# Optimization experiments

Measured on AMD Instinct MI355X. Metric: run time of the kernel, lower is better.

Reference implementation:

```python
import jax, jax.numpy as jnp
import numpy as np

N_GROUP = 8
TOPK_GROUP = 4
TOP_K = 8
ROUTED_SCALING_FACTOR = 2.5
RENORMALIZE = True


def setup_inputs() -> dict:
    key = jax.random.key(0)
    k1, k2 = jax.random.split(key)
    num_tokens, n_experts = 131072, 256
    router_logits = jax.random.normal(k1, (num_tokens, n_experts), dtype=jnp.float32)
    e_score_correction_bias = jax.random.normal(k2, (n_experts,), dtype=jnp.float32) * 0.1
    return {"router_logits": router_logits,
            "e_score_correction_bias": e_score_correction_bias}


def reference(router_logits, e_score_correction_bias):
    T, E = router_logits.shape
    per_group = E // N_GROUP  # 32 experts per group

    # sigmoid scoring + bias correction (bias used for selection only)
    scores = jax.nn.sigmoid(router_logits)                      # [T, E]
    scores_for_choice = scores + e_score_correction_bias[None, :]

    # group score = sum of top-2 corrected scores within each group
    grouped = scores_for_choice.reshape(T, N_GROUP, per_group)  # [T, G, E/G]
    top2_vals, _ = jax.lax.top_k(grouped, 2)                    # [T, G, 2]
    group_scores = top2_vals.sum(axis=-1)                       # [T, G]

    # pick topk_group groups, build expert-level mask
    _, group_idx = jax.lax.top_k(group_scores, TOPK_GROUP)      # [T, topk_group]
    group_mask = jnp.zeros((T, N_GROUP), dtype=jnp.bool_)
    group_mask = group_mask.at[jnp.arange(T)[:, None], group_idx].set(True)
    score_mask = jnp.repeat(group_mask, per_group, axis=1)      # [T, E]

    # mask non-selected groups, then global top-k over remaining experts
    masked_scores = jnp.where(score_mask, scores_for_choice, 0.0)
    _, topk_ids = jax.lax.top_k(masked_scores, TOP_K)           # [T, top_k]

    # gather UNcorrected sigmoid scores as weights
    topk_weights = jnp.take_along_axis(scores, topk_ids, axis=1)  # [T, top_k]
    if RENORMALIZE:
        topk_weights = topk_weights / (topk_weights.sum(axis=-1, keepdims=True) + 1e-20)
    topk_weights = topk_weights * ROUTED_SCALING_FACTOR
    return topk_weights, topk_ids
```

## Files before the change

kernel.cpp:

```cpp
#include <hip/hip_runtime.h>
#include <math.h>

#define THREADS 256
#define TPB 32
#define NEXP 256
#define Q_EPS  12u
#define QG_EPS 28u

__device__ __forceinline__ float fsigmoid(float x) {
    float e = __expf(-x);
    return __fdividef(1.0f, 1.0f + e);
}

__device__ __forceinline__ double dsigmoid(float xf) {
    xf = fminf(fmaxf(xf, -500.0f), 500.0f);
    double x = (double)xf;
    double t = x * -1.4426950408889634074;
    double n = floor(t + 0.5);
    int ni = (int)n;
    double u = (t - n) * 0.69314718055994530942;
    double pp = 2.08767569878680990e-9;
    pp = fma(pp, u, 2.50521083854417188e-8);
    pp = fma(pp, u, 2.75573192239858907e-7);
    pp = fma(pp, u, 2.75573192239858883e-6);
    pp = fma(pp, u, 2.48015873015873016e-5);
    pp = fma(pp, u, 1.98412698412698413e-4);
    pp = fma(pp, u, 1.38888888888888889e-3);
    pp = fma(pp, u, 8.33333333333333333e-3);
    pp = fma(pp, u, 4.16666666666666667e-2);
    pp = fma(pp, u, 1.66666666666666667e-1);
    pp = fma(pp, u, 0.5);
    pp = fma(pp, u, 1.0);
    pp = fma(pp, u, 1.0);
    double sc = __longlong_as_double((long long)(1023 + ni) << 52);
    double e = pp * sc;
    double w = 1.0 + e;
    double y = (double)__fdividef(1.0f, (float)w);
    y = fma(y, fma(-w, y, 1.0), y);
    y = fma(y, fma(-w, y, 1.0), y);
    return y;
}

#define DINS(cc, ee) do {                                                \
    double _d=(cc); int _e=(ee);                                         \
    if (_d > s7) {                                                       \
        bool _b0=_d>s0,_b1=_d>s1,_b2=_d>s2,_b3=_d>s3,_b4=_d>s4,          \
             _b5=_d>s5,_b6=_d>s6;                                        \
        s7=_b6?s6:_d;           c7=_b6?c6:_e;                            \
        s6=_b5?s5:(_b6?_d:s6);  c6=_b5?c5:(_b6?_e:c6);                   \
        s5=_b4?s4:(_b5?_d:s5);  c5=_b4?c4:(_b5?_e:c5);                   \
        s4=_b3?s3:(_b4?_d:s4);  c4=_b3?c3:(_b4?_e:c4);                   \
        s3=_b2?s2:(_b3?_d:s3);  c3=_b2?c2:(_b3?_e:c3);                   \
        s2=_b1?s1:(_b2?_d:s2);  c2=_b1?c1:(_b2?_e:c2);                   \
        s1=_b0?s0:(_b1?_d:s1);  c1=_b0?c0:(_b1?_e:c1);                   \
        s0=_b0?_d:s0;           c0=_b0?_e:c0;                            \
    } } while (0)


#define CEU(a, b) do {                                                   \
    unsigned _x=(a), _y=(b);                                             \
    (a) = _x>_y ? _x : _y; (b) = _x>_y ? _y : _x;                        \
} while (0)
#define VMU(a, b) do { (a) = (a)>(b) ? (a) : (b); } while (0)

#define SORT8U(v0,v1,v2,v3,v4,v5,v6,v7) do {                             \
    CEU(v0,v1); CEU(v2,v3); CEU(v4,v5); CEU(v6,v7);                      \
    CEU(v0,v2); CEU(v1,v3); CEU(v4,v6); CEU(v5,v7);                      \
    CEU(v1,v2); CEU(v5,v6);                                              \
    CEU(v0,v4); CEU(v1,v5); CEU(v2,v6); CEU(v3,v7);                      \
    CEU(v2,v4); CEU(v3,v5);                                              \
    CEU(v1,v2); CEU(v3,v4); CEU(v5,v6);                                  \
} while (0)

#define CLEAN9M(a0,a1,a2,a3,a4,a5,a6,a7,a8) do {                         \
    CEU(a0,a8);                                                          \
    CEU(a1,a5); CEU(a2,a6); CEU(a3,a7); CEU(a4,a8);                      \
    CEU(a1,a3); CEU(a2,a4); CEU(a5,a7); CEU(a6,a8);                      \
    CEU(a1,a2); CEU(a3,a4); CEU(a5,a6); CEU(a7,a8);                      \
} while (0)

#define XMERGE_U(d) do {                                                 \
    unsigned q0=(unsigned)__shfl_xor((int)m0,d,64),                      \
             q1=(unsigned)__shfl_xor((int)m1,d,64),                      \
             q2=(unsigned)__shfl_xor((int)m2,d,64),                      \
             q3=(unsigned)__shfl_xor((int)m3,d,64),                      \
             q4=(unsigned)__shfl_xor((int)m4,d,64),                      \
             q5=(unsigned)__shfl_xor((int)m5,d,64),                      \
             q6=(unsigned)__shfl_xor((int)m6,d,64),                      \
             q7=(unsigned)__shfl_xor((int)m7,d,64),                      \
             q8=(unsigned)__shfl_xor((int)m8,d,64);                      \
    VMU(m0,q8); VMU(m1,q7); VMU(m2,q6); VMU(m3,q5); VMU(m4,q4);          \
    VMU(m5,q3); VMU(m6,q2); VMU(m7,q1); VMU(m8,q0);                      \
    CLEAN9M(m0,m1,m2,m3,m4,m5,m6,m7,m8);                                 \
} while (0)

__global__ __launch_bounds__(THREADS, 4)
void noauxtc_router_kernel(const float* __restrict__ logits,
                           const float* __restrict__ bias,
                           float* __restrict__ out,
                           int T)
{
    __shared__ __align__(16) float bias_sh[NEXP];
    __shared__ __align__(16) float biasq_sh[NEXP];

    const int tid   = threadIdx.x;
    const int h     = tid & 7;
    const int p     = tid >> 3;
    const int tok0  = blockIdx.x * TPB;
    const int token = tok0 + p;
    const int lane  = tid & 63;
    const int base  = lane & 56;

    const float4* lg4 = (const float4*)logits;
    float4 st[8];
    #pragma unroll
    for (int k = 0; k < 8; ++k)
        st[k] = lg4[(size_t)token * 64 + h * 8 + k];

    {
        float b = bias[tid];
        bias_sh[tid]  = b;
        biasq_sh[tid] = fmaf(b, 4194304.0f, 2097152.0f);
    }
    __syncthreads();

    const float4* bq4 = (const float4*)biasq_sh;

    unsigned kk[32];
    #pragma unroll
    for (int q = 0; q < 8; ++q) {
        float4 Bq = bq4[h * 8 + q];
        float4 x  = st[q];
        int idf = 255 - (h * 32 + q * 4);
        kk[q*4+0] = ((unsigned)fmaf(fsigmoid(x.x), 4194304.0f, Bq.x) << 8) + (unsigned)(idf    );
        kk[q*4+1] = ((unsigned)fmaf(fsigmoid(x.y), 4194304.0f, Bq.y) << 8) + (unsigned)(idf - 1);
        kk[q*4+2] = ((unsigned)fmaf(fsigmoid(x.z), 4194304.0f, Bq.z) << 8) + (unsigned)(idf - 2);
        kk[q*4+3] = ((unsigned)fmaf(fsigmoid(x.w), 4194304.0f, Bq.w) << 8) + (unsigned)(idf - 3);
    }

    SORT8U(kk[0], kk[1], kk[2], kk[3], kk[4], kk[5], kk[6], kk[7]);
    SORT8U(kk[8], kk[9], kk[10],kk[11],kk[12],kk[13],kk[14],kk[15]);
    SORT8U(kk[16],kk[17],kk[18],kk[19],kk[20],kk[21],kk[22],kk[23]);
    SORT8U(kk[24],kk[25],kk[26],kk[27],kk[28],kk[29],kk[30],kk[31]);

    unsigned t0=kk[0],t1=kk[1],t2=kk[2],t3=kk[3],t4=kk[4],t5=kk[5],t6=kk[6],t7=kk[7],t8=0u;
    VMU(t1,kk[15]); VMU(t2,kk[14]); VMU(t3,kk[13]); VMU(t4,kk[12]);
    VMU(t5,kk[11]); VMU(t6,kk[10]); VMU(t7,kk[9]);  VMU(t8,kk[8]);
    CLEAN9M(t0,t1,t2,t3,t4,t5,t6,t7,t8);

    unsigned u0=kk[16],u1=kk[17],u2=kk[18],u3=kk[19],u4=kk[20],u5=kk[21],u6=kk[22],u7=kk[23],u8=0u;
    VMU(u1,kk[31]); VMU(u2,kk[30]); VMU(u3,kk[29]); VMU(u4,kk[28]);
    VMU(u5,kk[27]); VMU(u6,kk[26]); VMU(u7,kk[25]); VMU(u8,kk[24]);
    CLEAN9M(u0,u1,u2,u3,u4,u5,u6,u7,u8);

    unsigned m0=t0,m1=t1,m2=t2,m3=t3,m4=t4,m5=t5,m6=t6,m7=t7,m8=t8;
    VMU(m0,u8); VMU(m1,u7); VMU(m2,u6); VMU(m3,u5); VMU(m4,u4);
    VMU(m5,u3); VMU(m6,u2); VMU(m7,u1); VMU(m8,u0);
    CLEAN9M(m0,m1,m2,m3,m4,m5,m6,m7,m8);

    unsigned gq   = (m0 >> 8) + (m1 >> 8);
    unsigned gkey = (gq << 3) + (unsigned)(7 - h);

    unsigned gk0 = (unsigned)__shfl((int)gkey, base + 0, 64);
    unsigned gk1 = (unsigned)__shfl((int)gkey, base + 1, 64);
    unsigned gk2 = (unsigned)__shfl((int)gkey, base + 2, 64);
    unsigned gk3 = (unsigned)__shfl((int)gkey, base + 3, 64);
    unsigned gk4 = (unsigned)__shfl((int)gkey, base + 4, 64);
    unsigned gk5 = (unsigned)__shfl((int)gkey, base + 5, 64);
    unsigned gk6 = (unsigned)__shfl((int)gkey, base + 6, 64);
    unsigned gk7 = (unsigned)__shfl((int)gkey, base + 7, 64);
    SORT8U(gk0,gk1,gk2,gk3,gk4,gk5,gk6,gk7);

    int selmask = (1 << ((gk0 & 7u) ^ 7u)) | (1 << ((gk1 & 7u) ^ 7u)) |
                  (1 << ((gk2 & 7u) ^ 7u)) | (1 << ((gk3 & 7u) ^ 7u));

    if (__builtin_expect((gk3 >> 3) - (gk4 >> 3) < QG_EPS, 0)) {
        double a1 = -1e300, a2 = -1e300;
        const float* lgp = logits + (size_t)token * 256 + h * 32;
        #pragma unroll 1
        for (int k = 0; k < 32; ++k) {
            double c = dsigmoid(lgp[k]) + (double)bias_sh[h * 32 + k];
            a2 = fmax(a2, fmin(a1, c)); a1 = fmax(a1, c);
        }
        double gdo = a1 + a2;
        double gd[8];
        #pragma unroll
        for (int g = 0; g < 8; ++g) gd[g] = __shfl(gdo, base + g, 64);
        int sm = 0;
        #pragma unroll
        for (int a = 0; a < 8; ++a) {
            int rk = 0;
            #pragma unroll
            for (int b = 0; b < 8; ++b) {
                if (b == a) continue;
                bool beat = (b < a) ? (gd[b] >= gd[a]) : (gd[b] > gd[a]);
                rk += beat ? 1 : 0;
            }
            sm |= (rk < 4) ? (1 << a) : 0;
        }
        selmask = sm;
    }

    {
        bool sel = (selmask >> h) & 1;
        m0 = sel ? m0 : 0u; m1 = sel ? m1 : 0u; m2 = sel ? m2 : 0u;
        m3 = sel ? m3 : 0u; m4 = sel ? m4 : 0u; m5 = sel ? m5 : 0u;
        m6 = sel ? m6 : 0u; m7 = sel ? m7 : 0u; m8 = sel ? m8 : 0u;
    }

    XMERGE_U(1);
    XMERGE_U(2);
    XMERGE_U(4);

    unsigned q0=m0>>8, q1=m1>>8, q2=m2>>8, q3=m3>>8, q4=m4>>8,
             q5=m5>>8, q6=m6>>8, q7=m7>>8, q8=m8>>8;
    int n0=255-(int)(m0&255u), n1=255-(int)(m1&255u), n2=255-(int)(m2&255u),
        n3=255-(int)(m3&255u), n4=255-(int)(m4&255u), n5=255-(int)(m5&255u),
        n6=255-(int)(m6&255u), n7=255-(int)(m7&255u), n8=255-(int)(m8&255u);

    const float QS = 2.384185791015625e-7f;
    float v0=(float)q0*QS-0.5f, v1=(float)q1*QS-0.5f, v2=(float)q2*QS-0.5f,
          v3=(float)q3*QS-0.5f, v4=(float)q4*QS-0.5f, v5=(float)q5*QS-0.5f,
          v6=(float)q6*QS-0.5f, v7=(float)q7*QS-0.5f;

    float w0 = v0 - bias_sh[n0], w1 = v1 - bias_sh[n1], w2 = v2 - bias_sh[n2],
          w3 = v3 - bias_sh[n3], w4 = v4 - bias_sh[n4], w5 = v5 - bias_sh[n5],
          w6 = v6 - bias_sh[n6], w7 = v7 - bias_sh[n7];
    int o0=n0,o1=n1,o2=n2,o3=n3,o4=n4,o5=n5,o6=n6,o7=n7;

    bool flagB = (h == 0) &&
                 ((q0-q1<Q_EPS)|(q1-q2<Q_EPS)|(q2-q3<Q_EPS)|(q3-q4<Q_EPS)|
                  (q4-q5<Q_EPS)|(q5-q6<Q_EPS)|(q6-q7<Q_EPS)|(q7-q8<Q_EPS));
    if (__builtin_expect(flagB, 0)) {
        double s0=-1e300,s1=-1e300,s2=-1e300,s3=-1e300,
               s4=-1e300,s5=-1e300,s6=-1e300,s7=-1e300;
        int c0=0,c1=0,c2=0,c3=0,c4=0,c5=0,c6=0,c7=0;
        int ci[9] = {n0,n1,n2,n3,n4,n5,n6,n7,n8};
        const float* lgt = logits + (size_t)token * 256;
        #pragma unroll 1
        for (int k = 0; k < 9; ++k) {
            int e = ci[k];
            double cs = dsigmoid(lgt[e]) + (double)bias_sh[e];
            DINS(cs, e);
        }
        w0=(float)(s0-(double)bias_sh[c0]); o0=c0;
        w1=(float)(s1-(double)bias_sh[c1]); o1=c1;
        w2=(float)(s2-(double)bias_sh[c2]); o2=c2;
        w3=(float)(s3-(double)bias_sh[c3]); o3=c3;
        w4=(float)(s4-(double)bias_sh[c4]); o4=c4;
        w5=(float)(s5-(double)bias_sh[c5]); o5=c5;
        w6=(float)(s6-(double)bias_sh[c6]); o6=c6;
        w7=(float)(s7-(double)bias_sh[c7]); o7=c7;
    }

    if (h == 0) {
        float sum = ((w0+w1)+(w2+w3)) + ((w4+w5)+(w6+w7));
        float scl = 2.5f / (sum + 1e-20f);
        float4 oa, ob;
        oa.x=w0*scl; oa.y=w1*scl; oa.z=w2*scl; oa.w=w3*scl;
        ob.x=w4*scl; ob.y=w5*scl; ob.z=w6*scl; ob.w=w7*scl;
        *(float4*)(out + (size_t)token*8)     = oa;
        *(float4*)(out + (size_t)token*8 + 4) = ob;
        float* oid = out + (size_t)T*8;
        float4 ia, ib;
        ia.x=(float)o0; ia.y=(float)o1; ia.z=(float)o2; ia.w=(float)o3;
        ib.x=(float)o4; ib.y=(float)o5; ib.z=(float)o6; ib.w=(float)o7;
        *(float4*)(oid + (size_t)token*8)     = ia;
        *(float4*)(oid + (size_t)token*8 + 4) = ib;
    }
}

extern "C" void kernel_launch(void* const* d_in, const int* in_sizes, int n_in,
                              void* d_out, int out_size, void* d_ws, size_t ws_size,
                              hipStream_t stream) {
    const float* logits = (const float*)d_in[0];
    const float* bias   = (const float*)d_in[1];
    float* out = (float*)d_out;
    int T = in_sizes[0] / NEXP;
    int nblocks = T / TPB;
    noauxtc_router_kernel<<<nblocks, THREADS, 0, stream>>>(logits, bias, out, T);
}
```

Measured before the change: 200.6 us.

## Process two tokens per thread and drop shared-memory bias staging

Each block now handles 64 tokens, with every thread processing two tokens in sequence. This halves the grid and amortizes the per-block bias setup. The shared-memory bias arrays and the __syncthreads are removed. Each thread instead loads its 32 bias values into registers and prequantizes them once, and final bias lookups come from global memory (likely cached). The trade-offs are that the two tokens are processed serially without overlapping their loads, register pressure rises from holding the bias registers, and the number of blocks in flight drops.

```diff
diff --git a/kernel.cpp b/kernel.cpp
--- a/kernel.cpp
+++ b/kernel.cpp
@@ -2,7 +2,7 @@
 #include <math.h>
 
 #define THREADS 256
-#define TPB 32
+#define TPB 64
 #define NEXP 256
 #define Q_EPS  12u
 #define QG_EPS 28u
@@ -100,174 +100,175 @@
                            float* __restrict__ out,
                            int T)
 {
-    __shared__ __align__(16) float bias_sh[NEXP];
-    __shared__ __align__(16) float biasq_sh[NEXP];
-
     const int tid   = threadIdx.x;
     const int h     = tid & 7;
     const int p     = tid >> 3;
     const int tok0  = blockIdx.x * TPB;
-    const int token = tok0 + p;
     const int lane  = tid & 63;
     const int base  = lane & 56;
 
-    const float4* lg4 = (const float4*)logits;
-    float4 st[8];
+    const float4* bg4 = (const float4*)bias + h * 8;
+    float4 Bq[8];
     #pragma unroll
-    for (int k = 0; k < 8; ++k)
-        st[k] = lg4[(size_t)token * 64 + h * 8 + k];
-
-    {
-        float b = bias[tid];
-        bias_sh[tid]  = b;
-        biasq_sh[tid] = fmaf(b, 4194304.0f, 2097152.0f);
+    for (int j = 0; j < 8; ++j) {
+        float4 b = bg4[j];
+        Bq[j].x = fmaf(b.x, 4194304.0f, 2097152.0f);
+        Bq[j].y = fmaf(b.y, 4194304.0f, 2097152.0f);
+        Bq[j].z = fmaf(b.z, 4194304.0f, 2097152.0f);
+        Bq[j].w = fmaf(b.w, 4194304.0f, 2097152.0f);
     }
-    __syncthreads();
-
-    const float4* bq4 = (const float4*)biasq_sh;
-
-    unsigned kk[32];
-    #pragma unroll
-    for (int q = 0; q < 8; ++q) {
-        float4 Bq = bq4[h * 8 + q];
-        float4 x  = st[q];
-        int idf = 255 - (h * 32 + q * 4);
-        kk[q*4+0] = ((unsigned)fmaf(fsigmoid(x.x), 4194304.0f, Bq.x) << 8) + (unsigned)(idf    );
-        kk[q*4+1] = ((unsigned)fmaf(fsigmoid(x.y), 4194304.0f, Bq.y) << 8) + (unsigned)(idf - 1);
-        kk[q*4+2] = ((unsigned)fmaf(fsigmoid(x.z), 4194304.0f, Bq.z) << 8) + (unsigned)(idf - 2);
-        kk[q*4+3] = ((unsigned)fmaf(fsigmoid(x.w), 4194304.0f, Bq.w) << 8) + (unsigned)(idf - 3);
-    }
-
-    SORT8U(kk[0], kk[1], kk[2], kk[3], kk[4], kk[5], kk[6], kk[7]);
-    SORT8U(kk[8], kk[9], kk[10],kk[11],kk[12],kk[13],kk[14],kk[15]);
-    SORT8U(kk[16],kk[17],kk[18],kk[19],kk[20],kk[21],kk[22],kk[23]);
-    SORT8U(kk[24],kk[25],kk[26],kk[27],kk[28],kk[29],kk[30],kk[31]);
-
-    unsigned t0=kk[0],t1=kk[1],t2=kk[2],t3=kk[3],t4=kk[4],t5=kk[5],t6=kk[6],t7=kk[7],t8=0u;
-    VMU(t1,kk[15]); VMU(t2,kk[14]); VMU(t3,kk[13]); VMU(t4,kk[12]);
-    VMU(t5,kk[11]); VMU(t6,kk[10]); VMU(t7,kk[9]);  VMU(t8,kk[8]);
-    CLEAN9M(t0,t1,t2,t3,t4,t5,t6,t7,t8);
-
-    unsigned u0=kk[16],u1=kk[17],u2=kk[18],u3=kk[19],u4=kk[20],u5=kk[21],u6=kk[22],u7=kk[23],u8=0u;
-    VMU(u1,kk[31]); VMU(u2,kk[30]); VMU(u3,kk[29]); VMU(u4,kk[28]);
-    VMU(u5,kk[27]); VMU(u6,kk[26]); VMU(u7,kk[25]); VMU(u8,kk[24]);
-    CLEAN9M(u0,u1,u2,u3,u4,u5,u6,u7,u8);
-
-    unsigned m0=t0,m1=t1,m2=t2,m3=t3,m4=t4,m5=t5,m6=t6,m7=t7,m8=t8;
-    VMU(m0,u8); VMU(m1,u7); VMU(m2,u6); VMU(m3,u5); VMU(m4,u4);
-    VMU(m5,u3); VMU(m6,u2); VMU(m7,u1); VMU(m8,u0);
-    CLEAN9M(m0,m1,m2,m3,m4,m5,m6,m7,m8);
-
-    unsigned gq   = (m0 >> 8) + (m1 >> 8);
-    unsigned gkey = (gq << 3) + (unsigned)(7 - h);
-
-    unsigned gk0 = (unsigned)__shfl((int)gkey, base + 0, 64);
-    unsigned gk1 = (unsigned)__shfl((int)gkey, base + 1, 64);
-    unsigned gk2 = (unsigned)__shfl((int)gkey, base + 2, 64);
-    unsigned gk3 = (unsigned)__shfl((int)gkey, base + 3, 64);
-    unsigned gk4 = (unsigned)__shfl((int)gkey, base + 4, 64);
-    unsigned gk5 = (unsigned)__shfl((int)gkey, base + 5, 64);
-    unsigned gk6 = (unsigned)__shfl((int)gkey, base + 6, 64);
-    unsigned gk7 = (unsigned)__shfl((int)gkey, base + 7, 64);
-    SORT8U(gk0,gk1,gk2,gk3,gk4,gk5,gk6,gk7);
-
-    int selmask = (1 << ((gk0 & 7u) ^ 7u)) | (1 << ((gk1 & 7u) ^ 7u)) |
-                  (1 << ((gk2 & 7u) ^ 7u)) | (1 << ((gk3 & 7u) ^ 7u));
-
-    if (__builtin_expect((gk3 >> 3) - (gk4 >> 3) < QG_EPS, 0)) {
-        double a1 = -1e300, a2 = -1e300;
-        const float* lgp = logits + (size_t)token * 256 + h * 32;
-        #pragma unroll 1
-        for (int k = 0; k < 32; ++k) {
-            double c = dsigmoid(lgp[k]) + (double)bias_sh[h * 32 + k];
-            a2 = fmax(a2, fmin(a1, c)); a1 = fmax(a1, c);
-        }
-        double gdo = a1 + a2;
-        double gd[8];
+
+    auto process = [&](int token) {
+        const float4* lg4 = (const float4*)logits + (size_t)token * 64 + h * 8;
+        float4 st[8];
         #pragma unroll
-        for (int g = 0; g < 8; ++g) gd[g] = __shfl(gdo, base + g, 64);
-        int sm = 0;
+        for (int k = 0; k < 8; ++k) st[k] = lg4[k];
+
+        unsigned kk[32];
         #pragma unroll
-        for (int a = 0; a < 8; ++a) {
-            int rk = 0;
+        for (int q = 0; q < 8; ++q) {
+            float4 x = st[q], B = Bq[q];
+            int idf = 255 - (h * 32 + q * 4);
+            kk[q*4+0] = ((unsigned)fmaf(fsigmoid(x.x), 4194304.0f, B.x) << 8) + (unsigned)(idf    );
+            kk[q*4+1] = ((unsigned)fmaf(fsigmoid(x.y), 4194304.0f, B.y) << 8) + (unsigned)(idf - 1);
+            kk[q*4+2] = ((unsigned)fmaf(fsigmoid(x.z), 4194304.0f, B.z) << 8) + (unsigned)(idf - 2);
+            kk[q*4+3] = ((unsigned)fmaf(fsigmoid(x.w), 4194304.0f, B.w) << 8) + (unsigned)(idf - 3);
+        }
+
+        SORT8U(kk[0], kk[1], kk[2], kk[3], kk[4], kk[5], kk[6], kk[7]);
+        SORT8U(kk[8], kk[9], kk[10],kk[11],kk[12],kk[13],kk[14],kk[15]);
+        SORT8U(kk[16],kk[17],kk[18],kk[19],kk[20],kk[21],kk[22],kk[23]);
+        SORT8U(kk[24],kk[25],kk[26],kk[27],kk[28],kk[29],kk[30],kk[31]);
+
+        unsigned t0=kk[0],t1=kk[1],t2=kk[2],t3=kk[3],t4=kk[4],t5=kk[5],t6=kk[6],t7=kk[7],t8=0u;
+        VMU(t1,kk[15]); VMU(t2,kk[14]); VMU(t3,kk[13]); VMU(t4,kk[12]);
+        VMU(t5,kk[11]); VMU(t6,kk[10]); VMU(t7,kk[9]);  VMU(t8,kk[8]);
+        CLEAN9M(t0,t1,t2,t3,t4,t5,t6,t7,t8);
+
+        unsigned u0=kk[16],u1=kk[17],u2=kk[18],u3=kk[19],u4=kk[20],u5=kk[21],u6=kk[22],u7=kk[23],u8=0u;
+        VMU(u1,kk[31]); VMU(u2,kk[30]); VMU(u3,kk[29]); VMU(u4,kk[28]);
+        VMU(u5,kk[27]); VMU(u6,kk[26]); VMU(u7,kk[25]); VMU(u8,kk[24]);
+        CLEAN9M(u0,u1,u2,u3,u4,u5,u6,u7,u8);
+
+        unsigned m0=t0,m1=t1,m2=t2,m3=t3,m4=t4,m5=t5,m6=t6,m7=t7,m8=t8;
+        VMU(m0,u8); VMU(m1,u7); VMU(m2,u6); VMU(m3,u5); VMU(m4,u4);
+        VMU(m5,u3); VMU(m6,u2); VMU(m7,u1); VMU(m8,u0);
+        CLEAN9M(m0,m1,m2,m3,m4,m5,m6,m7,m8);
+
+        unsigned gq   = (m0 >> 8) + (m1 >> 8);
+        unsigned gkey = (gq << 3) + (unsigned)(7 - h);
+
+        unsigned gk0 = (unsigned)__shfl((int)gkey, base + 0, 64);
+        unsigned gk1 = (unsigned)__shfl((int)gkey, base + 1, 64);
+        unsigned gk2 = (unsigned)__shfl((int)gkey, base + 2, 64);
+        unsigned gk3 = (unsigned)__shfl((int)gkey, base + 3, 64);
+        unsigned gk4 = (unsigned)__shfl((int)gkey, base + 4, 64);
+        unsigned gk5 = (unsigned)__shfl((int)gkey, base + 5, 64);
+        unsigned gk6 = (unsigned)__shfl((int)gkey, base + 6, 64);
+        unsigned gk7 = (unsigned)__shfl((int)gkey, base + 7, 64);
+        SORT8U(gk0,gk1,gk2,gk3,gk4,gk5,gk6,gk7);
+
+        int selmask = (1 << ((gk0 & 7u) ^ 7u)) | (1 << ((gk1 & 7u) ^ 7u)) |
+                      (1 << ((gk2 & 7u) ^ 7u)) | (1 << ((gk3 & 7u) ^ 7u));
+
+        if (__builtin_expect((gk3 >> 3) - (gk4 >> 3) < QG_EPS, 0)) {
+            double a1 = -1e300, a2 = -1e300;
+            const float* lgp = logits + (size_t)token * 256 + h * 32;
+            const float* bp  = bias + h * 32;
+            #pragma unroll 1
+            for (int k = 0; k < 32; ++k) {
+                double c = dsigmoid(lgp[k]) + (double)bp[k];
+                a2 = fmax(a2, fmin(a1, c)); a1 = fmax(a1, c);
+            }
+            double gdo = a1 + a2;
+            double gd[8];
             #pragma unroll
-            for (int b = 0; b < 8; ++b) {
-                if (b == a) continue;
-                bool beat = (b < a) ? (gd[b] >= gd[a]) : (gd[b] > gd[a]);
-                rk += beat ? 1 : 0;
+            for (int g = 0; g < 8; ++g) gd[g] = __shfl(gdo, base + g, 64);
+            int sm = 0;
+            #pragma unroll
+            for (int a = 0; a < 8; ++a) {
+                int rk = 0;
+                #pragma unroll
+                for (int b = 0; b < 8; ++b) {
+                    if (b == a) continue;
+                    bool beat = (b < a) ? (gd[b] >= gd[a]) : (gd[b] > gd[a]);
+                    rk += beat ? 1 : 0;
+                }
+                sm |= (rk < 4) ? (1 << a) : 0;
             }
-            sm |= (rk < 4) ? (1 << a) : 0;
-        }
-        selmask = sm;
-    }
-
-    {
-        bool sel = (selmask >> h) & 1;
-        m0 = sel ? m0 : 0u; m1 = sel ? m1 : 0u; m2 = sel ? m2 : 0u;
-        m3 = sel ? m3 : 0u; m4 = sel ? m4 : 0u; m5 = sel ? m5 : 0u;
-        m6 = sel ? m6 : 0u; m7 = sel ? m7 : 0u; m8 = sel ? m8 : 0u;
-    }
-
-    XMERGE_U(1);
-    XMERGE_U(2);
-    XMERGE_U(4);
-
-    unsigned q0=m0>>8, q1=m1>>8, q2=m2>>8, q3=m3>>8, q4=m4>>8,
-             q5=m5>>8, q6=m6>>8, q7=m7>>8, q8=m8>>8;
-    int n0=255-(int)(m0&255u), n1=255-(int)(m1&255u), n2=255-(int)(m2&255u),
-        n3=255-(int)(m3&255u), n4=255-(int)(m4&255u), n5=255-(int)(m5&255u),
-        n6=255-(int)(m6&255u), n7=255-(int)(m7&255u), n8=255-(int)(m8&255u);
-
-    const float QS = 2.384185791015625e-7f;
-    float v0=(float)q0*QS-0.5f, v1=(float)q1*QS-0.5f, v2=(float)q2*QS-0.5f,
-          v3=(float)q3*QS-0.5f, v4=(float)q4*QS-0.5f, v5=(float)q5*QS-0.5f,
-          v6=(float)q6*QS-0.5f, v7=(float)q7*QS-0.5f;
-
-    float w0 = v0 - bias_sh[n0], w1 = v1 - bias_sh[n1], w2 = v2 - bias_sh[n2],
-          w3 = v3 - bias_sh[n3], w4 = v4 - bias_sh[n4], w5 = v5 - bias_sh[n5],
-          w6 = v6 - bias_sh[n6], w7 = v7 - bias_sh[n7];
-    int o0=n0,o1=n1,o2=n2,o3=n3,o4=n4,o5=n5,o6=n6,o7=n7;
-
-    bool flagB = (h == 0) &&
-                 ((q0-q1<Q_EPS)|(q1-q2<Q_EPS)|(q2-q3<Q_EPS)|(q3-q4<Q_EPS)|
-                  (q4-q5<Q_EPS)|(q5-q6<Q_EPS)|(q6-q7<Q_EPS)|(q7-q8<Q_EPS));
-    if (__builtin_expect(flagB, 0)) {
-        double s0=-1e300,s1=-1e300,s2=-1e300,s3=-1e300,
-               s4=-1e300,s5=-1e300,s6=-1e300,s7=-1e300;
-        int c0=0,c1=0,c2=0,c3=0,c4=0,c5=0,c6=0,c7=0;
-        int ci[9] = {n0,n1,n2,n3,n4,n5,n6,n7,n8};
-        const float* lgt = logits + (size_t)token * 256;
-        #pragma unroll 1
-        for (int k = 0; k < 9; ++k) {
-            int e = ci[k];
-            double cs = dsigmoid(lgt[e]) + (double)bias_sh[e];
-            DINS(cs, e);
-        }
-        w0=(float)(s0-(double)bias_sh[c0]); o0=c0;
-        w1=(float)(s1-(double)bias_sh[c1]); o1=c1;
-        w2=(float)(s2-(double)bias_sh[c2]); o2=c2;
-        w3=(float)(s3-(double)bias_sh[c3]); o3=c3;
-        w4=(float)(s4-(double)bias_sh[c4]); o4=c4;
-        w5=(float)(s5-(double)bias_sh[c5]); o5=c5;
-        w6=(float)(s6-(double)bias_sh[c6]); o6=c6;
-        w7=(float)(s7-(double)bias_sh[c7]); o7=c7;
-    }
-
-    if (h == 0) {
-        float sum = ((w0+w1)+(w2+w3)) + ((w4+w5)+(w6+w7));
-        float scl = 2.5f / (sum + 1e-20f);
-        float4 oa, ob;
-        oa.x=w0*scl; oa.y=w1*scl; oa.z=w2*scl; oa.w=w3*scl;
-        ob.x=w4*scl; ob.y=w5*scl; ob.z=w6*scl; ob.w=w7*scl;
-        *(float4*)(out + (size_t)token*8)     = oa;
-        *(float4*)(out + (size_t)token*8 + 4) = ob;
-        float* oid = out + (size_t)T*8;
-        float4 ia, ib;
-        ia.x=(float)o0; ia.y=(float)o1; ia.z=(float)o2; ia.w=(float)o3;
-        ib.x=(float)o4; ib.y=(float)o5; ib.z=(float)o6; ib.w=(float)o7;
-        *(float4*)(oid + (size_t)token*8)     = ia;
-        *(float4*)(oid + (size_t)token*8 + 4) = ib;
-    }
+            selmask = sm;
+        }
+
+        {
+            bool sel = (selmask >> h) & 1;
+            m0 = sel ? m0 : 0u; m1 = sel ? m1 : 0u; m2 = sel ? m2 : 0u;
+            m3 = sel ? m3 : 0u; m4 = sel ? m4 : 0u; m5 = sel ? m5 : 0u;
+            m6 = sel ? m6 : 0u; m7 = sel ? m7 : 0u; m8 = sel ? m8 : 0u;
+        }
+
+        XMERGE_U(1);
+        XMERGE_U(2);
+        XMERGE_U(4);
+
+        if (h == 0) {
+            unsigned q0=m0>>8, q1=m1>>8, q2=m2>>8, q3=m3>>8, q4=m4>>8,
+                     q5=m5>>8, q6=m6>>8, q7=m7>>8, q8=m8>>8;
+            int n0=255-(int)(m0&255u), n1=255-(int)(m1&255u), n2=255-(int)(m2&255u),
+                n3=255-(int)(m3&255u), n4=255-(int)(m4&255u), n5=255-(int)(m5&255u),
+                n6=255-(int)(m6&255u), n7=255-(int)(m7&255u), n8=255-(int)(m8&255u);
+
+            float bn0=bias[n0], bn1=bias[n1], bn2=bias[n2], bn3=bias[n3],
+                  bn4=bias[n4], bn5=bias[n5], bn6=bias[n6], bn7=bias[n7];
+
+            const float QS = 2.384185791015625e-7f;
+            float w0=fmaf((float)q0,QS,-0.5f)-bn0, w1=fmaf((float)q1,QS,-0.5f)-bn1,
+                  w2=fmaf((float)q2,QS,-0.5f)-bn2, w3=fmaf((float)q3,QS,-0.5f)-bn3,
+                  w4=fmaf((float)q4,QS,-0.5f)-bn4, w5=fmaf((float)q5,QS,-0.5f)-bn5,
+                  w6=fmaf((float)q6,QS,-0.5f)-bn6, w7=fmaf((float)q7,QS,-0.5f)-bn7;
+            int o0=n0,o1=n1,o2=n2,o3=n3,o4=n4,o5=n5,o6=n6,o7=n7;
+
+            bool flagB = ((q0-q1<Q_EPS)|(q1-q2<Q_EPS)|(q2-q3<Q_EPS)|(q3-q4<Q_EPS)|
+                          (q4-q5<Q_EPS)|(q5-q6<Q_EPS)|(q6-q7<Q_EPS)|(q7-q8<Q_EPS));
+            if (__builtin_expect(flagB, 0)) {
+                double s0=-1e300,s1=-1e300,s2=-1e300,s3=-1e300,
+                       s4=-1e300,s5=-1e300,s6=-1e300,s7=-1e300;
+                int c0=0,c1=0,c2=0,c3=0,c4=0,c5=0,c6=0,c7=0;
+                int ci[9] = {n0,n1,n2,n3,n4,n5,n6,n7,n8};
+                const float* lgt = logits + (size_t)token * 256;
+                #pragma unroll 1
+                for (int k = 0; k < 9; ++k) {
+                    int e = ci[k];
+                    double cs = dsigmoid(lgt[e]) + (double)bias[e];
+                    DINS(cs, e);
+                }
+                w0=(float)(s0-(double)bias[c0]); o0=c0;
+                w1=(float)(s1-(double)bias[c1]); o1=c1;
+                w2=(float)(s2-(double)bias[c2]); o2=c2;
+                w3=(float)(s3-(double)bias[c3]); o3=c3;
+                w4=(float)(s4-(double)bias[c4]); o4=c4;
+                w5=(float)(s5-(double)bias[c5]); o5=c5;
+                w6=(float)(s6-(double)bias[c6]); o6=c6;
+                w7=(float)(s7-(double)bias[c7]); o7=c7;
+            }
+
+            float sum = ((w0+w1)+(w2+w3)) + ((w4+w5)+(w6+w7));
+            float scl = 2.5f / (sum + 1e-20f);
+            float4 oa, ob;
+            oa.x=w0*scl; oa.y=w1*scl; oa.z=w2*scl; oa.w=w3*scl;
+            ob.x=w4*scl; ob.y=w5*scl; ob.z=w6*scl; ob.w=w7*scl;
+            *(float4*)(out + (size_t)token*8)     = oa;
+            *(float4*)(out + (size_t)token*8 + 4) = ob;
+            float* oid = out + (size_t)T*8;
+            float4 ia, ib;
+            ia.x=(float)o0; ia.y=(float)o1; ia.z=(float)o2; ia.w=(float)o3;
+            ib.x=(float)o4; ib.y=(float)o5; ib.z=(float)o6; ib.w=(float)o7;
+            *(float4*)(oid + (size_t)token*8)     = ia;
+            *(float4*)(oid + (size_t)token*8 + 4) = ib;
+        }
+    };
+
+    process(tok0 + p);
+    process(tok0 + 32 + p);
 }
 
 extern "C" void kernel_launch(void* const* d_in, const int* in_sizes, int n_in,
```

Measured after the change: 212.5 us. 5.9% more time.

## Stage logits through swizzled LDS tile for coalesced loads and rare-path reuse

Applied to the files above, without the earlier changes.

Global loads of logits switch from a per-thread strided pattern (each thread reading 128 contiguous bytes of its token) to fully coalesced block-wide float4 loads. The tile goes into a 32KB XOR-swizzled shared-memory buffer. Each thread then reads its group slice from LDS, and the double-precision fallback paths re-read logits from LDS instead of global memory. The weight/output epilogue is also moved inside the h==0 branch. The cost is the extra LDS traffic and 32KB of shared memory per block, which may limit occupancy under the launch bound of 4 blocks.

```diff
diff --git a/kernel.cpp b/kernel.cpp
--- a/kernel.cpp
+++ b/kernel.cpp
@@ -100,28 +100,37 @@
                            float* __restrict__ out,
                            int T)
 {
+    __shared__ float4 tile4[TPB * 64];
     __shared__ __align__(16) float bias_sh[NEXP];
     __shared__ __align__(16) float biasq_sh[NEXP];
 
     const int tid   = threadIdx.x;
     const int h     = tid & 7;
     const int p     = tid >> 3;
+    const int pm    = p & 7;
     const int tok0  = blockIdx.x * TPB;
     const int token = tok0 + p;
     const int lane  = tid & 63;
     const int base  = lane & 56;
 
     const float4* lg4 = (const float4*)logits;
-    float4 st[8];
+    float4 stg[8];
     #pragma unroll
     for (int k = 0; k < 8; ++k)
-        st[k] = lg4[(size_t)token * 64 + h * 8 + k];
+        stg[k] = lg4[(size_t)tok0 * 64 + k * 256 + tid];
 
     {
         float b = bias[tid];
         bias_sh[tid]  = b;
         biasq_sh[tid] = fmaf(b, 4194304.0f, 2097152.0f);
     }
+
+    #pragma unroll
+    for (int k = 0; k < 8; ++k) {
+        int flat = k * 256 + tid;
+        int t = flat >> 6, c = flat & 63;
+        tile4[t * 64 + (c ^ (t & 7))] = stg[k];
+    }
     __syncthreads();
 
     const float4* bq4 = (const float4*)biasq_sh;
@@ -129,13 +138,13 @@
     unsigned kk[32];
     #pragma unroll
     for (int q = 0; q < 8; ++q) {
-        float4 Bq = bq4[h * 8 + q];
-        float4 x  = st[q];
+        float4 x = tile4[p * 64 + ((h * 8 + q) ^ pm)];
+        float4 B = bq4[h * 8 + q];
         int idf = 255 - (h * 32 + q * 4);
-        kk[q*4+0] = ((unsigned)fmaf(fsigmoid(x.x), 4194304.0f, Bq.x) << 8) + (unsigned)(idf    );
-        kk[q*4+1] = ((unsigned)fmaf(fsigmoid(x.y), 4194304.0f, Bq.y) << 8) + (unsigned)(idf - 1);
-        kk[q*4+2] = ((unsigned)fmaf(fsigmoid(x.z), 4194304.0f, Bq.z) << 8) + (unsigned)(idf - 2);
-        kk[q*4+3] = ((unsigned)fmaf(fsigmoid(x.w), 4194304.0f, Bq.w) << 8) + (unsigned)(idf - 3);
+        kk[q*4+0] = ((unsigned)fmaf(fsigmoid(x.x), 4194304.0f, B.x) << 8) + (unsigned)(idf    );
+        kk[q*4+1] = ((unsigned)fmaf(fsigmoid(x.y), 4194304.0f, B.y) << 8) + (unsigned)(idf - 1);
+        kk[q*4+2] = ((unsigned)fmaf(fsigmoid(x.z), 4194304.0f, B.z) << 8) + (unsigned)(idf - 2);
+        kk[q*4+3] = ((unsigned)fmaf(fsigmoid(x.w), 4194304.0f, B.w) << 8) + (unsigned)(idf - 3);
     }
 
     SORT8U(kk[0], kk[1], kk[2], kk[3], kk[4], kk[5], kk[6], kk[7]);
@@ -176,10 +185,11 @@
 
     if (__builtin_expect((gk3 >> 3) - (gk4 >> 3) < QG_EPS, 0)) {
         double a1 = -1e300, a2 = -1e300;
-        const float* lgp = logits + (size_t)token * 256 + h * 32;
         #pragma unroll 1
         for (int k = 0; k < 32; ++k) {
-            double c = dsigmoid(lgp[k]) + (double)bias_sh[h * 32 + k];
+            int e = h * 32 + k;
+            const float* tf = (const float*)(tile4 + p * 64 + ((e >> 2) ^ pm));
+            double c = dsigmoid(tf[e & 3]) + (double)bias_sh[e];
             a2 = fmax(a2, fmin(a1, c)); a1 = fmax(a1, c);
         }
         double gdo = a1 + a2;
@@ -212,48 +222,47 @@
     XMERGE_U(2);
     XMERGE_U(4);
 
-    unsigned q0=m0>>8, q1=m1>>8, q2=m2>>8, q3=m3>>8, q4=m4>>8,
-             q5=m5>>8, q6=m6>>8, q7=m7>>8, q8=m8>>8;
-    int n0=255-(int)(m0&255u), n1=255-(int)(m1&255u), n2=255-(int)(m2&255u),
-        n3=255-(int)(m3&255u), n4=255-(int)(m4&255u), n5=255-(int)(m5&255u),
-        n6=255-(int)(m6&255u), n7=255-(int)(m7&255u), n8=255-(int)(m8&255u);
-
-    const float QS = 2.384185791015625e-7f;
-    float v0=(float)q0*QS-0.5f, v1=(float)q1*QS-0.5f, v2=(float)q2*QS-0.5f,
-          v3=(float)q3*QS-0.5f, v4=(float)q4*QS-0.5f, v5=(float)q5*QS-0.5f,
-          v6=(float)q6*QS-0.5f, v7=(float)q7*QS-0.5f;
-
-    float w0 = v0 - bias_sh[n0], w1 = v1 - bias_sh[n1], w2 = v2 - bias_sh[n2],
-          w3 = v3 - bias_sh[n3], w4 = v4 - bias_sh[n4], w5 = v5 - bias_sh[n5],
-          w6 = v6 - bias_sh[n6], w7 = v7 - bias_sh[n7];
-    int o0=n0,o1=n1,o2=n2,o3=n3,o4=n4,o5=n5,o6=n6,o7=n7;
-
-    bool flagB = (h == 0) &&
-                 ((q0-q1<Q_EPS)|(q1-q2<Q_EPS)|(q2-q3<Q_EPS)|(q3-q4<Q_EPS)|
-                  (q4-q5<Q_EPS)|(q5-q6<Q_EPS)|(q6-q7<Q_EPS)|(q7-q8<Q_EPS));
-    if (__builtin_expect(flagB, 0)) {
-        double s0=-1e300,s1=-1e300,s2=-1e300,s3=-1e300,
-               s4=-1e300,s5=-1e300,s6=-1e300,s7=-1e300;
-        int c0=0,c1=0,c2=0,c3=0,c4=0,c5=0,c6=0,c7=0;
-        int ci[9] = {n0,n1,n2,n3,n4,n5,n6,n7,n8};
-        const float* lgt = logits + (size_t)token * 256;
-        #pragma unroll 1
-        for (int k = 0; k < 9; ++k) {
-            int e = ci[k];
-            double cs = dsigmoid(lgt[e]) + (double)bias_sh[e];
-            DINS(cs, e);
+    if (h == 0) {
+        unsigned q0=m0>>8, q1=m1>>8, q2=m2>>8, q3=m3>>8, q4=m4>>8,
+                 q5=m5>>8, q6=m6>>8, q7=m7>>8, q8=m8>>8;
+        int n0=255-(int)(m0&255u), n1=255-(int)(m1&255u), n2=255-(int)(m2&255u),
+            n3=255-(int)(m3&255u), n4=255-(int)(m4&255u), n5=255-(int)(m5&255u),
+            n6=255-(int)(m6&255u), n7=255-(int)(m7&255u), n8=255-(int)(m8&255u);
+
+        float bn0=bias_sh[n0], bn1=bias_sh[n1], bn2=bias_sh[n2], bn3=bias_sh[n3],
+              bn4=bias_sh[n4], bn5=bias_sh[n5], bn6=bias_sh[n6], bn7=bias_sh[n7];
+
+        const float QS = 2.384185791015625e-7f;
+        float w0=fmaf((float)q0,QS,-0.5f)-bn0, w1=fmaf((float)q1,QS,-0.5f)-bn1,
+              w2=fmaf((float)q2,QS,-0.5f)-bn2, w3=fmaf((float)q3,QS,-0.5f)-bn3,
+              w4=fmaf((float)q4,QS,-0.5f)-bn4, w5=fmaf((float)q5,QS,-0.5f)-bn5,
+              w6=fmaf((float)q6,QS,-0.5f)-bn6, w7=fmaf((float)q7,QS,-0.5f)-bn7;
+        int o0=n0,o1=n1,o2=n2,o3=n3,o4=n4,o5=n5,o6=n6,o7=n7;
+
+        bool flagB = ((q0-q1<Q_EPS)|(q1-q2<Q_EPS)|(q2-q3<Q_EPS)|(q3-q4<Q_EPS)|
+                      (q4-q5<Q_EPS)|(q5-q6<Q_EPS)|(q6-q7<Q_EPS)|(q7-q8<Q_EPS));
+        if (__builtin_expect(flagB, 0)) {
+            double s0=-1e300,s1=-1e300,s2=-1e300,s3=-1e300,
+                   s4=-1e300,s5=-1e300,s6=-1e300,s7=-1e300;
+            int c0=0,c1=0,c2=0,c3=0,c4=0,c5=0,c6=0,c7=0;
+            int ci[9] = {n0,n1,n2,n3,n4,n5,n6,n7,n8};
+            #pragma unroll 1
+            for (int k = 0; k < 9; ++k) {
+                int e = ci[k];
+                const float* tf = (const float*)(tile4 + p * 64 + ((e >> 2) ^ pm));
+                double cs = dsigmoid(tf[e & 3]) + (double)bias_sh[e];
+                DINS(cs, e);
+            }
+            w0=(float)(s0-(double)bias_sh[c0]); o0=c0;
+            w1=(float)(s1-(double)bias_sh[c1]); o1=c1;
+            w2=(float)(s2-(double)bias_sh[c2]); o2=c2;
+            w3=(float)(s3-(double)bias_sh[c3]); o3=c3;
+            w4=(float)(s4-(double)bias_sh[c4]); o4=c4;
+            w5=(float)(s5-(double)bias_sh[c5]); o5=c5;
+            w6=(float)(s6-(double)bias_sh[c6]); o6=c6;
+            w7=(float)(s7-(double)bias_sh[c7]); o7=c7;
         }
-        w0=(float)(s0-(double)bias_sh[c0]); o0=c0;
-        w1=(float)(s1-(double)bias_sh[c1]); o1=c1;
-        w2=(float)(s2-(double)bias_sh[c2]); o2=c2;
-        w3=(float)(s3-(double)bias_sh[c3]); o3=c3;
-        w4=(float)(s4-(double)bias_sh[c4]); o4=c4;
-        w5=(float)(s5-(double)bias_sh[c5]); o5=c5;
-        w6=(float)(s6-(double)bias_sh[c6]); o6=c6;
-        w7=(float)(s7-(double)bias_sh[c7]); o7=c7;
-    }
-
-    if (h == 0) {
+
         float sum = ((w0+w1)+(w2+w3)) + ((w4+w5)+(w6+w7));
         float scl = 2.5f / (sum + 1e-20f);
         float4 oa, ob;
```

Result: no change. 197.7 us (-1.5%).
